# Kernel optimization log

Hardware: AMD Instinct MI355X
Metric: run time of the kernel (lower is better)

Reference implementation:

```python
import jax, jax.numpy as jnp
import numpy as np

NDIM = 3
RADIUS = 0.14
MAX_GRID_DIM = 96
MAX_COLLISIONS = 128
B, N, M, C = 4, 4096, 4096, 16


def setup_inputs() -> dict:
    key = jax.random.key(0)
    k1, k2, k3 = jax.random.split(key, 3)
    locs = jax.random.uniform(k1, (B, N, NDIM), dtype=jnp.float32)
    data = jax.random.normal(k2, (B, N, C), dtype=jnp.float32)
    qlocs = jax.random.uniform(k3, (B, M, NDIM), dtype=jnp.float32)
    return {"locs": locs, "data": data, "qlocs": qlocs}


def _hashgrid_idxs(locs, radius, max_grid_dim):
    """Replicates hashgrid_order: assign each particle a flat grid-cell ID and
    return the permutation (new -> old index) that sorts particles by cell."""
    lower = locs.min(axis=1)                                   # [B,D]
    upper = locs.max(axis=1)                                   # [B,D]
    grid_dims = jnp.ceil(jnp.clip((upper - lower) / radius, 0.0, max_grid_dim))
    center = (lower + upper) * 0.5
    lower = center - grid_dims * radius * 0.5                  # grid lower corner
    cell = jnp.floor((locs - lower[:, None, :]) / radius)
    cell = jnp.clip(cell, 0.0, grid_dims[:, None, :] - 1.0).astype(jnp.int32)
    gd = jnp.maximum(grid_dims.astype(jnp.int32), 1)           # [B,D]
    # row-major strides per batch: stride[d] = prod(gd[d+1:])
    rev = jnp.cumprod(gd[:, ::-1], axis=1)[:, ::-1]            # [B,D]
    strides = jnp.concatenate(
        [rev[:, 1:], jnp.ones((gd.shape[0], 1), jnp.int32)], axis=1)
    cell_ids = (cell * strides[:, None, :]).sum(-1)            # [B,N]
    # stable sort by cell id -> idxs[b, i] = original index of particle now at i
    idxs = jnp.argsort(cell_ids, axis=1)
    return idxs


def reference(locs, data, qlocs):
    idxs = _hashgrid_idxs(locs, RADIUS, MAX_GRID_DIM)
    locs_r = jnp.take_along_axis(locs, idxs[..., None], axis=1)   # [B,N,D]
    data_r = jnp.take_along_axis(data, idxs[..., None], axis=1)   # [B,N,C]

    # Radius search of qlocs against the cell-sorted particles. Neighbor indices
    # are w.r.t. the reordered locs, listed in ascending reordered-index order
    # (cell order), capped at MAX_COLLISIONS, padded with -1.
    qn = (qlocs * qlocs).sum(-1)                                  # [B,M]
    pn = (locs_r * locs_r).sum(-1)                                # [B,N]
    cross = jnp.einsum('bmd,bnd->bmn', qlocs, locs_r)             # [B,M,N]
    dist2 = qn[:, :, None] + pn[:, None, :] - 2.0 * cross         # [B,M,N]
    mask = dist2 <= RADIUS * RADIUS
    # stable argsort of ~mask puts in-radius particles first, in index order
    order = jnp.argsort(~mask, axis=-1)
    neighbors = order[..., :MAX_COLLISIONS].astype(jnp.int32)     # [B,M,K]
    count = mask.sum(-1)                                          # [B,M]
    valid = jnp.arange(MAX_COLLISIONS) < count[..., None]
    neighbors = jnp.where(valid, neighbors, jnp.int32(-1))
    return locs_r, data_r, idxs.astype(jnp.int32), neighbors
```

## Files before the change

kernel.cpp:

```cpp
#include <hip/hip_runtime.h>
#include <stdint.h>

#define BB 4
#define NN 4096
#define MM 4096
#define CC 16
#define KMAX 128

static constexpr int LOCSR_OFF = 0;
static constexpr int DATAR_OFF = BB * NN * 3;
static constexpr int IDXS_OFF  = DATAR_OFF + BB * NN * CC;
static constexpr int NB_OFF    = IDXS_OFF + BB * NN;

static constexpr float RAD_F = 0.14f;
static constexpr float R2F   = (float)(0.14 * 0.14);

static constexpr int MAXC    = 96 * 96 * 96;
static constexpr int CSTRIDE = MAXC + 8;

__global__ void __launch_bounds__(256) k_bbox(const float* __restrict__ locs,
                                              float* __restrict__ pmm) {
    int blk = blockIdx.x;
    int b = blk >> 4, s = blk & 15, t = threadIdx.x;
    int i = s * 256 + t;
    const float* p = locs + (b * NN + i) * 3;
    float x0 = p[0], x1 = p[1], x2 = p[2];
    __shared__ float sm[6][256];
    sm[0][t] = x0; sm[1][t] = x1; sm[2][t] = x2;
    sm[3][t] = x0; sm[4][t] = x1; sm[5][t] = x2;
    __syncthreads();
    for (int st = 128; st > 0; st >>= 1) {
        if (t < st) {
            sm[0][t] = fminf(sm[0][t], sm[0][t + st]);
            sm[1][t] = fminf(sm[1][t], sm[1][t + st]);
            sm[2][t] = fminf(sm[2][t], sm[2][t + st]);
            sm[3][t] = fmaxf(sm[3][t], sm[3][t + st]);
            sm[4][t] = fmaxf(sm[4][t], sm[4][t + st]);
            sm[5][t] = fmaxf(sm[5][t], sm[5][t + st]);
        }
        __syncthreads();
    }
    if (t == 0) {
        float* o = pmm + blk * 6;
        o[0] = sm[0][0]; o[1] = sm[1][0]; o[2] = sm[2][0];
        o[3] = sm[3][0]; o[4] = sm[4][0]; o[5] = sm[5][0];
    }
}

__global__ void __launch_bounds__(1024) k_rank(const float* __restrict__ locs,
                                               const float* __restrict__ data,
                                               const float* __restrict__ pmm,
                                               float* __restrict__ out,
                                               float4* __restrict__ sp4,
                                               unsigned* __restrict__ cs_sorted,
                                               float* __restrict__ gp) {
    __shared__ uint4 keys4[NN / 4];
    __shared__ int partial[16][64];
    __shared__ int s_dst[64];
    __shared__ float sp_low[3], sp_gdf[3];
    __shared__ int sp_s0, sp_s1;
    int blk = blockIdx.x;
    int b = blk >> 6;
    int t = threadIdx.x;
    int wave = t >> 6, lane = t & 63;

    if (t == 0) {
        const float* pm = pmm + b * 96;
        float mn0 = 1e30f, mn1 = 1e30f, mn2 = 1e30f;
        float mx0 = -1e30f, mx1 = -1e30f, mx2 = -1e30f;
#pragma unroll
        for (int k = 0; k < 16; ++k) {
            mn0 = fminf(mn0, pm[k * 6 + 0]);
            mn1 = fminf(mn1, pm[k * 6 + 1]);
            mn2 = fminf(mn2, pm[k * 6 + 2]);
            mx0 = fmaxf(mx0, pm[k * 6 + 3]);
            mx1 = fmaxf(mx1, pm[k * 6 + 4]);
            mx2 = fmaxf(mx2, pm[k * 6 + 5]);
        }
        float lo[3] = {mn0, mn1, mn2}, up[3] = {mx0, mx1, mx2};
        float low2[3], gdf[3];
        int gdi[3];
#pragma unroll
        for (int d = 0; d < 3; ++d) {
            float u = __fdiv_rn(__fsub_rn(up[d], lo[d]), RAD_F);
            u = fminf(fmaxf(u, 0.0f), 96.0f);
            float g = ceilf(u);
            float center = __fmul_rn(__fadd_rn(lo[d], up[d]), 0.5f);
            low2[d] = __fsub_rn(center, __fmul_rn(__fmul_rn(g, RAD_F), 0.5f));
            gdf[d] = g;
            gdi[d] = max((int)g, 1);
        }
        sp_low[0] = low2[0]; sp_low[1] = low2[1]; sp_low[2] = low2[2];
        sp_gdf[0] = gdf[0];  sp_gdf[1] = gdf[1];  sp_gdf[2] = gdf[2];
        sp_s0 = gdi[1] * gdi[2];
        sp_s1 = gdi[2];
        if ((blk & 63) == 0) {
            float* o = gp + b * 12;
            o[0] = low2[0]; o[1] = low2[1]; o[2] = low2[2];
            o[3] = gdf[0];  o[4] = gdf[1];  o[5] = gdf[2];
            ((int*)o)[6]  = gdi[1] * gdi[2];
            ((int*)o)[7]  = gdi[2];
            ((int*)o)[8]  = gdi[0] * gdi[1] * gdi[2];
            ((int*)o)[9]  = gdi[0];
            ((int*)o)[10] = gdi[1];
            ((int*)o)[11] = gdi[2];
        }
    }
    __syncthreads();

    {
        float l0 = sp_low[0], l1 = sp_low[1], l2 = sp_low[2];
        float g0 = sp_gdf[0], g1 = sp_gdf[1], g2 = sp_gdf[2];
        int s0 = sp_s0, s1 = sp_s1;
        const float4* lp = (const float4*)(locs + b * NN * 3) + t * 3;
        float4 A = lp[0], Bv = lp[1], Cv = lp[2];
        float ex[4] = {A.x, A.w, Bv.z, Cv.y};
        float ey[4] = {A.y, Bv.x, Bv.w, Cv.z};
        float ez[4] = {A.z, Bv.y, Cv.x, Cv.w};
        unsigned kk[4];
#pragma unroll
        for (int j = 0; j < 4; ++j) {
            float c0 = fminf(fmaxf(floorf(__fdiv_rn(__fsub_rn(ex[j], l0), RAD_F)), 0.0f), __fsub_rn(g0, 1.0f));
            float c1 = fminf(fmaxf(floorf(__fdiv_rn(__fsub_rn(ey[j], l1), RAD_F)), 0.0f), __fsub_rn(g1, 1.0f));
            float c2 = fminf(fmaxf(floorf(__fdiv_rn(__fsub_rn(ez[j], l2), RAD_F)), 0.0f), __fsub_rn(g2, 1.0f));
            unsigned cell = (unsigned)((int)c0 * s0 + (int)c1 * s1 + (int)c2);
            kk[j] = cell * 4096u + (unsigned)(4 * t + j);
        }
        keys4[t] = make_uint4(kk[0], kk[1], kk[2], kk[3]);
    }
    __syncthreads();

    int i = (blk & 63) * 64 + lane;
    unsigned key = ((const unsigned*)keys4)[i];
    uint4 mv = keys4[wave * 64 + lane];
    int rank = 0;
#pragma unroll
    for (int s = 0; s < 64; ++s) {
        unsigned a  = (unsigned)__builtin_amdgcn_readlane((int)mv.x, s);
        unsigned b2 = (unsigned)__builtin_amdgcn_readlane((int)mv.y, s);
        unsigned c2 = (unsigned)__builtin_amdgcn_readlane((int)mv.z, s);
        unsigned d2 = (unsigned)__builtin_amdgcn_readlane((int)mv.w, s);
        rank += (int)(a < key) + (int)(b2 < key) + (int)(c2 < key) + (int)(d2 < key);
    }
    partial[wave][lane] = rank;
    __syncthreads();
    if (wave == 0) {
        int r = 0;
#pragma unroll
        for (int w = 0; w < 16; ++w) r += partial[w][lane];
        s_dst[lane] = r;
    }
    __syncthreads();
    if (wave == 0) {
        int src = b * NN + i;
        int dst = b * NN + s_dst[lane];
        float x = locs[src * 3 + 0], y = locs[src * 3 + 1], z = locs[src * 3 + 2];
        out[IDXS_OFF + dst] = (float)i;
        out[LOCSR_OFF + dst * 3 + 0] = x;
        out[LOCSR_OFF + dst * 3 + 1] = y;
        out[LOCSR_OFF + dst * 3 + 2] = z;
        cs_sorted[dst] = key;
        float pn = __fadd_rn(__fadd_rn(__fmul_rn(x, x), __fmul_rn(y, y)), __fmul_rn(z, z));
        sp4[dst] = make_float4(x, y, z, pn);
    } else if (wave <= 4) {
        int p = lane;
        int ii = (blk & 63) * 64 + p;
        int dst = b * NN + s_dst[p];
        int c = wave - 1;
        const float4* dsrc = (const float4*)(data + (b * NN + ii) * 16);
        float4* ddst = (float4*)(out + DATAR_OFF + dst * 16);
        ddst[c] = dsrc[c];
    }
}

__global__ void __launch_bounds__(256) k_cellstart(const unsigned* __restrict__ cs_sorted,
                                                   const float* __restrict__ gp,
                                                   int* __restrict__ cell_start) {
    int b = blockIdx.y;
    int nc = ((const int*)(gp + b * 12))[8];
    const unsigned* cs = cs_sorted + b * NN;
    int* cst = cell_start + b * CSTRIDE;
    for (int c = blockIdx.x * 256 + threadIdx.x; c <= nc; c += gridDim.x * 256) {
        int lo = 0, hi = NN;
        while (lo < hi) {
            int mid = (lo + hi) >> 1;
            if ((int)(cs[mid] >> 12) < c) lo = mid + 1; else hi = mid;
        }
        cst[c] = lo;
    }
}

__device__ inline void axis_range(float qd, float lo, int gd, int* c0, int* c1) {
    const float DL = RAD_F + 1e-4f;
    float vlo = (qd - DL - lo) / RAD_F;
    float vhi = (qd + DL - lo) / RAD_F;
    int a = (int)floorf(vlo), b = (int)floorf(vhi);
    *c0 = min(max(a, 0), gd - 1);
    *c1 = min(max(b, 0), gd - 1);
}

__global__ void __launch_bounds__(256, 8) k_neighbors(const float* __restrict__ qlocs,
                                                      const float4* __restrict__ sp4,
                                                      const int* __restrict__ cell_start,
                                                      const float* __restrict__ gp,
                                                      float* __restrict__ out) {
    int blk = blockIdx.x;
    int b = blk >> 10;
    int wave = threadIdx.x >> 6, lane = threadIdx.x & 63;
    int m = (blk & 1023) * 4 + wave;
    const float* o = gp + b * 12;
    const int* oi = (const int*)o;
    int s0 = oi[6], s1 = oi[7];
    int gd0 = oi[9], gd1 = oi[10], gd2 = oi[11];
    const float* q = qlocs + (b * MM + m) * 3;
    float q0 = q[0], q1 = q[1], q2 = q[2];
    float qn = __fadd_rn(__fadd_rn(__fmul_rn(q0, q0), __fmul_rn(q1, q1)), __fmul_rn(q2, q2));
    int cx0, cx1, cy0, cy1, cz0, cz1;
    axis_range(q0, o[0], gd0, &cx0, &cx1);
    axis_range(q1, o[1], gd1, &cy0, &cy1);
    axis_range(q2, o[2], gd2, &cz0, &cz1);
    const float4* sp = sp4 + b * NN;
    const int* cst = cell_start + b * CSTRIDE;
    float* nb = out + NB_OFF + (b * MM + m) * KMAX;

    int psA[3][3], peA[3][3];
#pragma unroll
    for (int dx = 0; dx < 3; ++dx) {
#pragma unroll
        for (int dy = 0; dy < 3; ++dy) {
            int cx = cx0 + dx, cy = cy0 + dy;
            bool v = (cx <= cx1) && (cy <= cy1);
            int base = cx * s0 + cy * s1;
            int i0 = v ? base + cz0 : 0;
            int i1 = v ? base + cz1 + 1 : 0;
            int ps = cst[i0];
            int pe = cst[i1];
            psA[dx][dy] = v ? ps : 0;
            peA[dx][dy] = v ? pe : 0;
        }
    }

    int count = 0;
#pragma unroll
    for (int dx = 0; dx < 3; ++dx) {
#pragma unroll
        for (int dy = 0; dy < 3; ++dy) {
            int ps = psA[dx][dy], pe = peA[dx][dy];
            for (int p0 = ps; p0 < pe; p0 += 64) {
                int p = p0 + lane;
                float4 P = sp[p];
                float cross = fmaf(q2, P.z, fmaf(q1, P.y, __fmul_rn(q0, P.x)));
                float dist2 = __fsub_rn(__fadd_rn(qn, P.w), __fmul_rn(2.0f, cross));
                bool hit = (p < pe) && (dist2 <= R2F);
                unsigned long long bal = __ballot(hit);
                if (hit) {
                    int pos = count + __popcll(bal & ((1ull << lane) - 1ull));
                    if (pos < KMAX) nb[pos] = (float)p;
                }
                count += __popcll(bal);
            }
        }
    }
    for (int j = count + lane; j < KMAX; j += 64) nb[j] = -1.0f;
}

extern "C" void kernel_launch(void* const* d_in, const int* in_sizes, int n_in,
                              void* d_out, int out_size, void* d_ws, size_t ws_size,
                              hipStream_t stream) {
    const float* locs  = (const float*)d_in[0];
    const float* data  = (const float*)d_in[1];
    const float* qlocs = (const float*)d_in[2];
    float* out = (float*)d_out;
    char* ws = (char*)d_ws;
    float*    gp        = (float*)ws;
    float*    pmm       = (float*)(ws + 512);
    unsigned* cs_sorted = (unsigned*)(ws + 4608);
    float4*   sp4       = (float4*)(ws + 4608 + 65536);
    int* cell_start = (int*)(ws + 4608 + 65536 + BB * NN * sizeof(float4));

    k_bbox<<<BB * 16, 256, 0, stream>>>(locs, pmm);
    k_rank<<<BB * 64, 1024, 0, stream>>>(locs, data, pmm, out, sp4, cs_sorted, gp);
    k_cellstart<<<dim3(32, BB), 256, 0, stream>>>(cs_sorted, gp, cell_start);
    k_neighbors<<<BB * 1024, 256, 0, stream>>>(qlocs, sp4, cell_start, gp, out);
}
```

Before: 93.03 us.

## Flatten neighbor-cell ranges into one packed lane loop with early exit

```diff
diff --git a/kernel.cpp b/kernel.cpp
--- a/kernel.cpp
+++ b/kernel.cpp
@@ -199,7 +199,7 @@
     *c1 = min(max(b, 0), gd - 1);
 }
 
-__global__ void __launch_bounds__(256, 8) k_neighbors(const float* __restrict__ qlocs,
+__global__ void __launch_bounds__(256, 6) k_neighbors(const float* __restrict__ qlocs,
                                                       const float4* __restrict__ sp4,
                                                       const int* __restrict__ cell_start,
                                                       const float* __restrict__ gp,
@@ -223,43 +223,49 @@
     const int* cst = cell_start + b * CSTRIDE;
     float* nb = out + NB_OFF + (b * MM + m) * KMAX;
 
-    int psA[3][3], peA[3][3];
+    int ps_[9], pe_[9];
 #pragma unroll
     for (int dx = 0; dx < 3; ++dx) {
 #pragma unroll
         for (int dy = 0; dy < 3; ++dy) {
+            int k = dx * 3 + dy;
             int cx = cx0 + dx, cy = cy0 + dy;
             bool v = (cx <= cx1) && (cy <= cy1);
             int base = cx * s0 + cy * s1;
             int i0 = v ? base + cz0 : 0;
             int i1 = v ? base + cz1 + 1 : 0;
-            int ps = cst[i0];
-            int pe = cst[i1];
-            psA[dx][dy] = v ? ps : 0;
-            peA[dx][dy] = v ? pe : 0;
-        }
-    }
+            int a = cst[i0];
+            int e = cst[i1];
+            ps_[k] = v ? a : 0;
+            pe_[k] = v ? e : 0;
+        }
+    }
+    int pre_[10];
+    pre_[0] = 0;
+#pragma unroll
+    for (int k = 0; k < 9; ++k) pre_[k + 1] = pre_[k] + max(pe_[k] - ps_[k], 0);
+    int T = pre_[9];
 
     int count = 0;
-#pragma unroll
-    for (int dx = 0; dx < 3; ++dx) {
-#pragma unroll
-        for (int dy = 0; dy < 3; ++dy) {
-            int ps = psA[dx][dy], pe = peA[dx][dy];
-            for (int p0 = ps; p0 < pe; p0 += 64) {
-                int p = p0 + lane;
-                float4 P = sp[p];
-                float cross = fmaf(q2, P.z, fmaf(q1, P.y, __fmul_rn(q0, P.x)));
-                float dist2 = __fsub_rn(__fadd_rn(qn, P.w), __fmul_rn(2.0f, cross));
-                bool hit = (p < pe) && (dist2 <= R2F);
-                unsigned long long bal = __ballot(hit);
-                if (hit) {
-                    int pos = count + __popcll(bal & ((1ull << lane) - 1ull));
-                    if (pos < KMAX) nb[pos] = (float)p;
-                }
-                count += __popcll(bal);
-            }
-        }
+    for (int l0 = 0; l0 < T; l0 += 64) {
+        int l = l0 + lane;
+        int p = 0;
+#pragma unroll
+        for (int k = 0; k < 9; ++k) {
+            bool in = (l >= pre_[k]) && (l < pre_[k + 1]);
+            p = in ? (ps_[k] + (l - pre_[k])) : p;
+        }
+        float4 P = sp[p];
+        float cross = fmaf(q2, P.z, fmaf(q1, P.y, __fmul_rn(q0, P.x)));
+        float dist2 = __fsub_rn(__fadd_rn(qn, P.w), __fmul_rn(2.0f, cross));
+        bool hit = (l < T) && (dist2 <= R2F);
+        unsigned long long bal = __ballot(hit);
+        if (hit) {
+            int pos = count + __popcll(bal & ((1ull << lane) - 1ull));
+            if (pos < KMAX) nb[pos] = (float)p;
+        }
+        count += __popcll(bal);
+        if (count >= KMAX) break;
     }
     for (int j = count + lane; j < KMAX; j += 64) nb[j] = -1.0f;
 }
```

Result: no change. 93.72 us (+0.7%).
